# Performance work log

Hardware: AMD Instinct MI355X
Metric: run time of the kernel (lower is better)

Reference implementation:

```python
import jax, jax.numpy as jnp
import numpy as np

N = 50000          # nodes
E = 1600000        # edges (avg degree 32)
D_IN = 128
D_OUT = 128
NUM_ETYPES = 8
K = 10             # propagation hops
ALPHA = 0.1
EDGE_HID = 32


def setup_inputs() -> dict:
    key = jax.random.key(0)
    ks = jax.random.split(key, 14)
    def lin(k, fan_in, fan_out):
        lim = 1.0 / np.sqrt(fan_in)
        return jax.random.uniform(k, (fan_in, fan_out), jnp.float32, -lim, lim)
    return {
        "feat": jax.random.normal(ks[0], (N, D_IN), jnp.float32),
        "e_feat": jax.random.randint(ks[1], (E,), 0, NUM_ETYPES),
        "src": jax.random.randint(ks[2], (E,), 0, N),
        "dst": jax.random.randint(ks[3], (E,), 0, N),
        "edge_embeds": jax.random.normal(ks[4], (NUM_ETYPES, D_IN), jnp.float32),
        "We1": lin(ks[5], D_IN, EDGE_HID),
        "be1": jnp.zeros((EDGE_HID,), jnp.float32),
        "We2": lin(ks[6], EDGE_HID, 1),
        "be2": jnp.zeros((1,), jnp.float32),
        "W1": lin(ks[7], D_IN, D_OUT),
        "b1": jnp.zeros((D_OUT,), jnp.float32),
        "W2": lin(ks[8], D_OUT, D_OUT),
        "b2": jnp.zeros((D_OUT,), jnp.float32),
    }


def reference(feat, e_feat, src, dst, edge_embeds, We1, be1, We2, be2, W1, b1, W2, b2):
    # degree-based symmetric normalization (clamped at 1)
    ones_e = jnp.ones((E,), feat.dtype)
    out_deg = jax.ops.segment_sum(ones_e, src, num_segments=N)
    in_deg = jax.ops.segment_sum(ones_e, dst, num_segments=N)
    src_norm = jnp.power(jnp.maximum(out_deg, 1.0), -0.5)[:, None]  # [N,1]
    dst_norm = jnp.power(jnp.maximum(in_deg, 1.0), -0.5)[:, None]   # [N,1]

    # per-edge gate: sigmoid(MLP(embedding(etype)))  -> [E,1]
    eh = jax.nn.gelu(edge_embeds[e_feat] @ We1 + be1, approximate=False)
    e_gate = jax.nn.sigmoid(eh @ We2 + be2)
    w = 1.0 + e_gate  # edge_drop p=0 -> identity on the ones tensor

    feat_0 = feat

    def hop(h, _):
        h = h * src_norm                                   # [N,D]
        m = h[src] * w                                     # [E,D] gather + gate
        agg = jax.ops.segment_sum(m, dst, num_segments=N)  # [N,D] scatter-sum
        h = agg * dst_norm
        h = (1.0 - ALPHA) * h + ALPHA * feat_0             # residual mix
        return h, None

    feat, _ = jax.lax.scan(hop, feat, None, length=K)

    # output MLP: Linear -> GELU -> Linear
    return jax.nn.gelu(feat @ W1 + b1, approximate=False) @ W2 + b2
```

## Files before the change

kernel.cpp:

```cpp
#include <hip/hip_runtime.h>
#include <cmath>


#define NNODES 50000
#define NEDGES 1600000
#define DD 128
#define KHOPS 10
#define ALPHA 0.1f

#define RS 16384
#define NRANGE 4
#define NSLICE 64
#define SLICE_E (NEDGES / NSLICE)

typedef short short8 __attribute__((ext_vector_type(8)));
typedef float f32x4 __attribute__((ext_vector_type(4)));

static __device__ __forceinline__ unsigned bf16rne(float x) {
    unsigned u = __float_as_uint(x);
    return (u + 0x7FFFu + ((u >> 16) & 1u)) >> 16;
}
static __device__ __forceinline__ float bf_lo(unsigned w) { return __uint_as_float(w << 16); }
static __device__ __forceinline__ float bf_hi(unsigned w) { return __uint_as_float(w & 0xFFFF0000u); }

__global__ __launch_bounds__(256) void gate_kernel(const float* __restrict__ emb,
                                                   const float* __restrict__ We1,
                                                   const float* __restrict__ be1,
                                                   const float* __restrict__ We2,
                                                   const float* __restrict__ be2,
                                                   float* __restrict__ gate) {
    int tid = threadIdx.x;
    int t = tid >> 5, j = tid & 31;
    float a = be1[j];
#pragma unroll 8
    for (int k = 0; k < DD; k++)
        a += emb[t * DD + k] * We1[k * 32 + j];
    float g = 0.5f * a * (1.0f + erff(a * 0.70710678118654752f));
    float p = g * We2[j];
#pragma unroll
    for (int m = 16; m >= 1; m >>= 1) p += __shfl_xor(p, m, 32);
    if (j == 0) gate[t] = 1.0f + 1.0f / (1.0f + expf(-(p + be2[0])));
}

__global__ __launch_bounds__(256) void hist_kernel(const int* __restrict__ key,
                                                   int* __restrict__ cnt) {
    __shared__ int h[RS];
    int b = blockIdx.x, r = blockIdx.y;
    int lo = r * RS;
    int hi = lo + RS; if (hi > NNODES) hi = NNODES;
    for (int i = threadIdx.x; i < RS; i += 256) h[i] = 0;
    __syncthreads();
    const int4* p = (const int4*)(key + b * SLICE_E);
    for (int i = threadIdx.x; i < SLICE_E / 4; i += 256) {
        int4 v = p[i];
        if (v.x >= lo && v.x < hi) atomicAdd(&h[v.x - lo], 1);
        if (v.y >= lo && v.y < hi) atomicAdd(&h[v.y - lo], 1);
        if (v.z >= lo && v.z < hi) atomicAdd(&h[v.z - lo], 1);
        if (v.w >= lo && v.w < hi) atomicAdd(&h[v.w - lo], 1);
    }
    __syncthreads();
    int n = hi - lo;
    for (int i = threadIdx.x; i < n; i += 256)
        cnt[(size_t)b * NNODES + lo + i] = h[i];
}

__global__ __launch_bounds__(256) void reduce_kernel(const int* __restrict__ cnt_in,
                                                     const int* __restrict__ cnt_out,
                                                     int* __restrict__ incnt,
                                                     int* __restrict__ outcnt, int N) {
    int n = blockIdx.x * 256 + threadIdx.x;
    if (n >= N) return;
    int a = 0, b = 0;
    for (int x = 0; x < NSLICE; x++) {
        a += cnt_in[(size_t)x * NNODES + n];
        b += cnt_out[(size_t)x * NNODES + n];
    }
    incnt[n] = a;
    outcnt[n] = b;
}

__global__ __launch_bounds__(256) void scan1_kernel(const int* __restrict__ cnt,
                                                    int* __restrict__ excl,
                                                    int* __restrict__ bsum, int N) {
    __shared__ int sh[256];
    int t = threadIdx.x;
    int g = blockIdx.x * 256 + t;
    int v = (g < N) ? cnt[g] : 0;
    sh[t] = v;
    __syncthreads();
    for (int off = 1; off < 256; off <<= 1) {
        int u = 0;
        if (t >= off) u = sh[t - off];
        __syncthreads();
        sh[t] += u;
        __syncthreads();
    }
    if (g < N) excl[g] = sh[t] - v;
    if (t == 255) bsum[blockIdx.x] = sh[255];
}
__global__ __launch_bounds__(256) void scan2_kernel(int* __restrict__ bsum, int nb) {
    __shared__ int sh[256];
    int t = threadIdx.x;
    int v = (t < nb) ? bsum[t] : 0;
    sh[t] = v;
    __syncthreads();
    for (int off = 1; off < 256; off <<= 1) {
        int u = 0;
        if (t >= off) u = sh[t - off];
        __syncthreads();
        sh[t] += u;
        __syncthreads();
    }
    if (t < nb) bsum[t] = sh[t] - v;
}
__global__ __launch_bounds__(256) void scan3_kernel(const int* __restrict__ excl,
                                                    const int* __restrict__ bsum,
                                                    int* __restrict__ row_ptr, int N, int E) {
    int g = blockIdx.x * 256 + threadIdx.x;
    if (g < N) row_ptr[g] = excl[g] + bsum[g >> 8];
    if (g == N) row_ptr[N] = E;
}

__global__ __launch_bounds__(256) void base_kernel(const int* __restrict__ row_ptr,
                                                   const int* __restrict__ cnt_in,
                                                   int* __restrict__ base_part, int N) {
    int n = blockIdx.x * 256 + threadIdx.x;
    if (n >= N) return;
    int run = row_ptr[n];
    for (int b = 0; b < NSLICE; b++) {
        base_part[(size_t)b * NNODES + n] = run;
        run += cnt_in[(size_t)b * NNODES + n];
    }
}

__global__ __launch_bounds__(256) void scatter2_kernel(const int* __restrict__ src,
                                                       const int* __restrict__ dst,
                                                       const int* __restrict__ ef,
                                                       const int* __restrict__ base_part,
                                                       int* __restrict__ epay) {
    __shared__ int cur[RS];
    int b = blockIdx.x, r = blockIdx.y;
    int lo = r * RS;
    int hi = lo + RS; if (hi > NNODES) hi = NNODES;
    int n = hi - lo;
    for (int i = threadIdx.x; i < n; i += 256)
        cur[i] = base_part[(size_t)b * NNODES + lo + i];
    __syncthreads();
    int off = b * SLICE_E;
    const int4* pd = (const int4*)(dst + off);
    const int4* ps = (const int4*)(src + off);
    const int4* pf = (const int4*)(ef + off);
    for (int i = threadIdx.x; i < SLICE_E / 4; i += 256) {
        int4 d = pd[i];
        int4 s = ps[i];
        int4 f = pf[i];
        int dv[4] = {d.x, d.y, d.z, d.w};
        int sv[4] = {s.x, s.y, s.z, s.w};
        int fv[4] = {f.x, f.y, f.z, f.w};
#pragma unroll
        for (int u = 0; u < 4; u++) {
            if (dv[u] >= lo && dv[u] < hi) {
                int pos = atomicAdd(&cur[dv[u] - lo], 1);
                epay[pos] = sv[u] | (fv[u] << 16);
            }
        }
    }
}

__global__ void scale_kernel(const float* __restrict__ feat, const int* __restrict__ outcnt,
                             unsigned* __restrict__ g0, int N) {
    int i = blockIdx.x * blockDim.x + threadIdx.x;
    if (i >= N * 32) return;
    int row = i >> 5;
    int oc = outcnt[row]; if (oc < 1) oc = 1;
    float sn = rsqrtf((float)oc);
    float4 v = ((const float4*)feat)[i];
    uint2 o;
    o.x = bf16rne(v.x * sn) | (bf16rne(v.y * sn) << 16);
    o.y = bf16rne(v.z * sn) | (bf16rne(v.w * sn) << 16);
    ((uint2*)g0)[i] = o;
}

__global__ __launch_bounds__(256) void hop_kernel(const unsigned* __restrict__ g_in,
                                                  const float* __restrict__ feat0,
                                                  const int* __restrict__ incnt,
                                                  const int* __restrict__ outcnt,
                                                  const float* __restrict__ gate_g,
                                                  const int* __restrict__ row_ptr,
                                                  const int* __restrict__ epay,
                                                  unsigned* __restrict__ g_out,
                                                  int N, int last) {
    __shared__ float gateL[8];
    if (threadIdx.x < 8) gateL[threadIdx.x] = gate_g[threadIdx.x];
    __syncthreads();
    int half = threadIdx.x >> 5;
    int lane = threadIdx.x & 31;
    int node = blockIdx.x * 8 + half;
    if (node >= N) return;
    int beg = row_ptr[node], end = row_ptr[node + 1];
    const uint2* gp = (const uint2*)g_in;
    float a0 = 0.f, a1 = 0.f, a2 = 0.f, a3 = 0.f;
    for (int base = beg; base < end; base += 32) {
        int n = end - base; if (n > 32) n = 32;
        int p = 0;
        if (lane < n) p = epay[base + lane];
        int j = 0;
        for (; j + 8 <= n; j += 8) {
            int pj[8];
#pragma unroll
            for (int u = 0; u < 8; u++) pj[u] = __shfl(p, j + u, 32);
            uint2 v[8];
#pragma unroll
            for (int u = 0; u < 8; u++)
                v[u] = gp[(size_t)(pj[u] & 0xFFFF) * 32 + lane];
#pragma unroll
            for (int u = 0; u < 8; u++) {
                float c = gateL[(unsigned)pj[u] >> 16];
                a0 += c * bf_lo(v[u].x); a1 += c * bf_hi(v[u].x);
                a2 += c * bf_lo(v[u].y); a3 += c * bf_hi(v[u].y);
            }
        }
        for (; j < n; j++) {
            int pj = __shfl(p, j, 32);
            float c = gateL[(unsigned)pj >> 16];
            uint2 v = gp[(size_t)(pj & 0xFFFF) * 32 + lane];
            a0 += c * bf_lo(v.x); a1 += c * bf_hi(v.x);
            a2 += c * bf_lo(v.y); a3 += c * bf_hi(v.y);
        }
    }
    int ic = incnt[node]; if (ic < 1) ic = 1;
    float dn = rsqrtf((float)ic) * (1.0f - ALPHA);
    float4 fv = *(const float4*)(feat0 + (size_t)node * DD + lane * 4);
    float h0 = dn * a0 + ALPHA * fv.x;
    float h1 = dn * a1 + ALPHA * fv.y;
    float h2 = dn * a2 + ALPHA * fv.z;
    float h3 = dn * a3 + ALPHA * fv.w;
    float sc = 1.0f;
    if (!last) { int oc = outcnt[node]; if (oc < 1) oc = 1; sc = rsqrtf((float)oc); }
    uint2 o;
    o.x = bf16rne(h0 * sc) | (bf16rne(h1 * sc) << 16);
    o.y = bf16rne(h2 * sc) | (bf16rne(h3 * sc) << 16);
    ((uint2*)g_out)[(size_t)node * 32 + lane] = o;
}

#define ASTR 136
__global__ __launch_bounds__(256) void mlp_mfma_kernel(const unsigned short* __restrict__ in,
                                                       const float* __restrict__ W,
                                                       const float* __restrict__ bias,
                                                       void* __restrict__ outp,
                                                       int N, int mode) {
    __shared__ unsigned short As[64 * ASTR];
    __shared__ unsigned short Bs[128 * ASTR];
    int tid = threadIdx.x;
    int row0 = blockIdx.x * 64;
    for (int i = tid; i < 64 * 16; i += 256) {
        int r = i >> 4, c8 = i & 15;
        int gr = row0 + r; if (gr >= N) gr = N - 1;
        uint4 v = *(const uint4*)(in + (size_t)gr * DD + c8 * 8);
        *(uint4*)&As[r * ASTR + c8 * 8] = v;
    }
    for (int i = tid; i < 128 * 128; i += 256) {
        int k = i >> 7, n = i & 127;
        Bs[n * ASTR + k] = (unsigned short)bf16rne(W[i]);
    }
    __syncthreads();

    int wv = tid >> 6, lane = tid & 63;
    int m = lane & 15, quad = lane >> 4;
    const unsigned short* arow = &As[(16 * wv + m) * ASTR + quad * 8];
    f32x4 acc[8];
#pragma unroll
    for (int t = 0; t < 8; t++) {
        const unsigned short* brow = &Bs[(t * 16 + m) * ASTR + quad * 8];
        f32x4 c = {0.f, 0.f, 0.f, 0.f};
#pragma unroll
        for (int s = 0; s < 4; s++) {
            short8 a = *(const short8*)(arow + s * 32);
            short8 b = *(const short8*)(brow + s * 32);
            c = __builtin_amdgcn_mfma_f32_16x16x32_bf16(a, b, c, 0, 0, 0);
        }
        acc[t] = c;
    }
#pragma unroll
    for (int t = 0; t < 8; t++) {
        float bv = bias[t * 16 + m];
#pragma unroll
        for (int r = 0; r < 4; r++) {
            int grow = row0 + 16 * wv + quad * 4 + r;
            if (grow >= N) continue;
            float v = acc[t][r] + bv;
            size_t oidx = (size_t)grow * DD + t * 16 + m;
            if (mode == 0) {
                v = 0.5f * v * (1.0f + erff(v * 0.70710678118654752f));
                ((unsigned short*)outp)[oidx] = (unsigned short)bf16rne(v);
            } else {
                ((float*)outp)[oidx] = v;
            }
        }
    }
}

extern "C" void kernel_launch(void* const* d_in, const int* in_sizes, int n_in,
                              void* d_out, int out_size, void* d_ws, size_t ws_size,
                              hipStream_t stream) {
    const float* feat = (const float*)d_in[0];
    const int*   e_feat = (const int*)d_in[1];
    const int*   src = (const int*)d_in[2];
    const int*   dst = (const int*)d_in[3];
    const float* emb = (const float*)d_in[4];
    const float* We1 = (const float*)d_in[5];
    const float* be1 = (const float*)d_in[6];
    const float* We2 = (const float*)d_in[7];
    const float* be2 = (const float*)d_in[8];
    const float* W1  = (const float*)d_in[9];
    const float* b1  = (const float*)d_in[10];
    const float* W2  = (const float*)d_in[11];
    const float* b2  = (const float*)d_in[12];
    float* out = (float*)d_out;

    const int N = NNODES, E = NEDGES;
    const int NBLK = (N + 255) / 256;
    char* ws = (char*)d_ws;
    size_t off = 0;
    unsigned* ga = (unsigned*)(ws + off);  off += (size_t)N * 256;
    unsigned* gb = (unsigned*)(ws + off);  off += (size_t)N * 256;
    int*   epay = (int*)(ws + off);        off += (size_t)E * 4;
    int*   row_ptr = (int*)(ws + off);     off += (size_t)(N + 1) * 4;
    int*   excl = (int*)(ws + off);        off += (size_t)N * 4;
    int*   bsum = (int*)(ws + off);        off += 256 * 4;
    int*   cnts = (int*)(ws + off);        off += (size_t)2 * N * 4;
    int*   cnt_in = (int*)(ws + off);      off += (size_t)NSLICE * N * 4;
    int*   cnt_out = (int*)(ws + off);     off += (size_t)NSLICE * N * 4;
    int*   base_part = (int*)(ws + off);   off += (size_t)NSLICE * N * 4;
    float* gate = (float*)(ws + off);      off += 64;
    int* incnt  = cnts;
    int* outcnt = cnts + N;

    gate_kernel<<<1, 256, 0, stream>>>(emb, We1, be1, We2, be2, gate);
    dim3 hg(NSLICE, NRANGE);
    hist_kernel<<<hg, 256, 0, stream>>>(dst, cnt_in);
    hist_kernel<<<hg, 256, 0, stream>>>(src, cnt_out);
    reduce_kernel<<<(N + 255) / 256, 256, 0, stream>>>(cnt_in, cnt_out, incnt, outcnt, N);
    scan1_kernel<<<NBLK, 256, 0, stream>>>(incnt, excl, bsum, N);
    scan2_kernel<<<1, 256, 0, stream>>>(bsum, NBLK);
    scan3_kernel<<<(N + 256) / 256 + 1, 256, 0, stream>>>(excl, bsum, row_ptr, N, E);
    base_kernel<<<(N + 255) / 256, 256, 0, stream>>>(row_ptr, cnt_in, base_part, N);
    scatter2_kernel<<<hg, 256, 0, stream>>>(src, dst, e_feat, base_part, epay);
    scale_kernel<<<(N * 32 + 255) / 256, 256, 0, stream>>>(feat, outcnt, ga, N);

    const unsigned* gin = ga;
    unsigned* gout = gb;
    for (int k = 0; k < KHOPS; k++) {
        int last = (k == KHOPS - 1);
        hop_kernel<<<(N + 7) / 8, 256, 0, stream>>>(gin, feat, incnt, outcnt, gate,
                                                    row_ptr, epay, gout, N, last);
        gin = gout;
        gout = (gout == ga) ? gb : ga;
    }
    const unsigned short* hfin = (const unsigned short*)gin;
    unsigned short* hidden = (unsigned short*)gout;
    mlp_mfma_kernel<<<(N + 63) / 64, 256, 0, stream>>>(hfin, W1, b1, hidden, N, 0);
    mlp_mfma_kernel<<<(N + 63) / 64, 256, 0, stream>>>(hidden, W2, b2, out, N, 1);
}
```

Measured before the change: 769.8 us.

## Fuse reduce+scan, pre-convert MLP weights to bf16, deepen hop gather unroll

Merges the degree-reduction and first scan kernel into one launch, removing a launch and a read-back of incnt. Adds a small kernel that converts W1 and W2 to bf16 once, so the 782 MLP blocks no longer each reconvert the fp32 weights. The hop gather loop now issues 12 independent row loads per batch and uses 32-bit index math, to keep more memory requests in flight. The deeper unroll raises register pressure and could lower occupancy.

```diff
diff --git a/kernel.cpp b/kernel.cpp
--- a/kernel.cpp
+++ b/kernel.cpp
@@ -42,6 +42,17 @@
     if (j == 0) gate[t] = 1.0f + 1.0f / (1.0f + expf(-(p + be2[0])));
 }
 
+__global__ __launch_bounds__(256) void wconv_kernel(const float* __restrict__ W1,
+                                                    const float* __restrict__ W2,
+                                                    unsigned short* __restrict__ w1b,
+                                                    unsigned short* __restrict__ w2b) {
+    int i = blockIdx.x * 256 + threadIdx.x;
+    if (i < DD * DD) {
+        w1b[i] = (unsigned short)bf16rne(W1[i]);
+        w2b[i] = (unsigned short)bf16rne(W2[i]);
+    }
+}
+
 __global__ __launch_bounds__(256) void hist_kernel(const int* __restrict__ key,
                                                    int* __restrict__ cnt) {
     __shared__ int h[RS];
@@ -64,28 +75,25 @@
         cnt[(size_t)b * NNODES + lo + i] = h[i];
 }
 
-__global__ __launch_bounds__(256) void reduce_kernel(const int* __restrict__ cnt_in,
-                                                     const int* __restrict__ cnt_out,
-                                                     int* __restrict__ incnt,
-                                                     int* __restrict__ outcnt, int N) {
-    int n = blockIdx.x * 256 + threadIdx.x;
-    if (n >= N) return;
-    int a = 0, b = 0;
-    for (int x = 0; x < NSLICE; x++) {
-        a += cnt_in[(size_t)x * NNODES + n];
-        b += cnt_out[(size_t)x * NNODES + n];
-    }
-    incnt[n] = a;
-    outcnt[n] = b;
-}
-
-__global__ __launch_bounds__(256) void scan1_kernel(const int* __restrict__ cnt,
-                                                    int* __restrict__ excl,
-                                                    int* __restrict__ bsum, int N) {
+__global__ __launch_bounds__(256) void reduce_scan_kernel(const int* __restrict__ cnt_in,
+                                                          const int* __restrict__ cnt_out,
+                                                          int* __restrict__ incnt,
+                                                          int* __restrict__ outcnt,
+                                                          int* __restrict__ excl,
+                                                          int* __restrict__ bsum, int N) {
     __shared__ int sh[256];
     int t = threadIdx.x;
     int g = blockIdx.x * 256 + t;
-    int v = (g < N) ? cnt[g] : 0;
+    int a = 0, b = 0;
+    if (g < N) {
+        for (int x = 0; x < NSLICE; x++) {
+            a += cnt_in[(size_t)x * NNODES + g];
+            b += cnt_out[(size_t)x * NNODES + g];
+        }
+        incnt[g] = a;
+        outcnt[g] = b;
+    }
+    int v = a;
     sh[t] = v;
     __syncthreads();
     for (int off = 1; off < 256; off <<= 1) {
@@ -98,6 +106,7 @@
     if (g < N) excl[g] = sh[t] - v;
     if (t == 255) bsum[blockIdx.x] = sh[255];
 }
+
 __global__ __launch_bounds__(256) void scan2_kernel(int* __restrict__ bsum, int nb) {
     __shared__ int sh[256];
     int t = threadIdx.x;
@@ -205,25 +214,40 @@
         int p = 0;
         if (lane < n) p = epay[base + lane];
         int j = 0;
+        for (; j + 12 <= n; j += 12) {
+            float cg[12];
+            uint2 v[12];
+#pragma unroll
+            for (int u = 0; u < 12; u++) {
+                int pj = __shfl(p, j + u, 32);
+                cg[u] = gateL[(unsigned)pj >> 16];
+                v[u] = gp[((unsigned)(pj & 0xFFFF) << 5) + lane];
+            }
+#pragma unroll
+            for (int u = 0; u < 12; u++) {
+                a0 += cg[u] * bf_lo(v[u].x); a1 += cg[u] * bf_hi(v[u].x);
+                a2 += cg[u] * bf_lo(v[u].y); a3 += cg[u] * bf_hi(v[u].y);
+            }
+        }
         for (; j + 8 <= n; j += 8) {
-            int pj[8];
-#pragma unroll
-            for (int u = 0; u < 8; u++) pj[u] = __shfl(p, j + u, 32);
+            float cg[8];
             uint2 v[8];
 #pragma unroll
-            for (int u = 0; u < 8; u++)
-                v[u] = gp[(size_t)(pj[u] & 0xFFFF) * 32 + lane];
-#pragma unroll
             for (int u = 0; u < 8; u++) {
-                float c = gateL[(unsigned)pj[u] >> 16];
-                a0 += c * bf_lo(v[u].x); a1 += c * bf_hi(v[u].x);
-                a2 += c * bf_lo(v[u].y); a3 += c * bf_hi(v[u].y);
+                int pj = __shfl(p, j + u, 32);
+                cg[u] = gateL[(unsigned)pj >> 16];
+                v[u] = gp[((unsigned)(pj & 0xFFFF) << 5) + lane];
+            }
+#pragma unroll
+            for (int u = 0; u < 8; u++) {
+                a0 += cg[u] * bf_lo(v[u].x); a1 += cg[u] * bf_hi(v[u].x);
+                a2 += cg[u] * bf_lo(v[u].y); a3 += cg[u] * bf_hi(v[u].y);
             }
         }
         for (; j < n; j++) {
             int pj = __shfl(p, j, 32);
             float c = gateL[(unsigned)pj >> 16];
-            uint2 v = gp[(size_t)(pj & 0xFFFF) * 32 + lane];
+            uint2 v = gp[((unsigned)(pj & 0xFFFF) << 5) + lane];
             a0 += c * bf_lo(v.x); a1 += c * bf_hi(v.x);
             a2 += c * bf_lo(v.y); a3 += c * bf_hi(v.y);
         }
@@ -245,7 +269,7 @@
 
 #define ASTR 136
 __global__ __launch_bounds__(256) void mlp_mfma_kernel(const unsigned short* __restrict__ in,
-                                                       const float* __restrict__ W,
+                                                       const unsigned short* __restrict__ Wb,
                                                        const float* __restrict__ bias,
                                                        void* __restrict__ outp,
                                                        int N, int mode) {
@@ -261,7 +285,7 @@
     }
     for (int i = tid; i < 128 * 128; i += 256) {
         int k = i >> 7, n = i & 127;
-        Bs[n * ASTR + k] = (unsigned short)bf16rne(W[i]);
+        Bs[n * ASTR + k] = Wb[i];
     }
     __syncthreads();
 
@@ -332,16 +356,19 @@
     int*   cnt_in = (int*)(ws + off);      off += (size_t)NSLICE * N * 4;
     int*   cnt_out = (int*)(ws + off);     off += (size_t)NSLICE * N * 4;
     int*   base_part = (int*)(ws + off);   off += (size_t)NSLICE * N * 4;
+    unsigned short* w1b = (unsigned short*)(ws + off); off += (size_t)DD * DD * 2;
+    unsigned short* w2b = (unsigned short*)(ws + off); off += (size_t)DD * DD * 2;
     float* gate = (float*)(ws + off);      off += 64;
     int* incnt  = cnts;
     int* outcnt = cnts + N;
 
     gate_kernel<<<1, 256, 0, stream>>>(emb, We1, be1, We2, be2, gate);
+    wconv_kernel<<<(DD * DD + 255) / 256, 256, 0, stream>>>(W1, W2, w1b, w2b);
     dim3 hg(NSLICE, NRANGE);
     hist_kernel<<<hg, 256, 0, stream>>>(dst, cnt_in);
     hist_kernel<<<hg, 256, 0, stream>>>(src, cnt_out);
-    reduce_kernel<<<(N + 255) / 256, 256, 0, stream>>>(cnt_in, cnt_out, incnt, outcnt, N);
-    scan1_kernel<<<NBLK, 256, 0, stream>>>(incnt, excl, bsum, N);
+    reduce_scan_kernel<<<NBLK, 256, 0, stream>>>(cnt_in, cnt_out, incnt, outcnt,
+                                                 excl, bsum, N);
     scan2_kernel<<<1, 256, 0, stream>>>(bsum, NBLK);
     scan3_kernel<<<(N + 256) / 256 + 1, 256, 0, stream>>>(excl, bsum, row_ptr, N, E);
     base_kernel<<<(N + 255) / 256, 256, 0, stream>>>(row_ptr, cnt_in, base_part, N);
@@ -359,6 +386,6 @@
     }
     const unsigned short* hfin = (const unsigned short*)gin;
     unsigned short* hidden = (unsigned short*)gout;
-    mlp_mfma_kernel<<<(N + 63) / 64, 256, 0, stream>>>(hfin, W1, b1, hidden, N, 0);
-    mlp_mfma_kernel<<<(N + 63) / 64, 256, 0, stream>>>(hidden, W2, b2, out, N, 1);
-}
+    mlp_mfma_kernel<<<(N + 63) / 64, 256, 0, stream>>>(hfin, w1b, b1, hidden, N, 0);
+    mlp_mfma_kernel<<<(N + 63) / 64, 256, 0, stream>>>(hidden, w2b, b2, out, N, 1);
+}
```

Measured after the change: 776.9 us. Within noise of the previous version (+0.9%).
